# Kernel optimization log

Hardware: AMD Instinct MI355X
Metric: run time of the kernel (lower is better)

The kernel has to match this reference:

```python
import jax, jax.numpy as jnp
import numpy as np
import math

ATTN_TEMP = 1.0


def bilinear_sample(fea, gx, gy):
    """fea: [B,C,Hs,Ws]; gx, gy: [B,N] pixel coords (align_corners=True), zero padding."""
    B, C, Hs, Ws = fea.shape
    x0 = jnp.floor(gx)
    y0 = jnp.floor(gy)
    x1 = x0 + 1.0
    y1 = y0 + 1.0
    wx1 = gx - x0
    wx0 = 1.0 - wx1
    wy1 = gy - y0
    wy0 = 1.0 - wy1
    flat = fea.reshape(B, C, Hs * Ws)

    def gather(xi, yi, w):
        valid = (xi >= 0) & (xi <= Ws - 1) & (yi >= 0) & (yi <= Hs - 1)
        xi_c = jnp.clip(xi, 0, Ws - 1).astype(jnp.int32)
        yi_c = jnp.clip(yi, 0, Hs - 1).astype(jnp.int32)
        idx = yi_c * Ws + xi_c  # [B,N]
        vals = jnp.take_along_axis(flat, idx[:, None, :], axis=2)  # [B,C,N]
        return vals * (w * valid.astype(fea.dtype))[:, None, :]

    return (gather(x0, y0, wx0 * wy0) + gather(x1, y0, wx1 * wy0)
            + gather(x0, y1, wx0 * wy1) + gather(x1, y1, wx1 * wy1))


def homo_warp(src_fea, src_proj, ref_proj, depth_values):
    """Plane-sweep homography warp. src_fea [B,C,Hs,Ws], projs [B,4,4], depth [B,D,Hr,Wr]."""
    B, C, Hs, Ws = src_fea.shape
    _, D, Hr, Wr = depth_values.shape
    proj = src_proj @ jnp.linalg.inv(ref_proj)
    rot = proj[:, :3, :3]
    trans = proj[:, :3, 3]  # [B,3]
    y, x = jnp.meshgrid(jnp.arange(Hr, dtype=src_fea.dtype),
                        jnp.arange(Wr, dtype=src_fea.dtype), indexing='ij')
    ones = jnp.ones(Hr * Wr, dtype=src_fea.dtype)
    xyz = jnp.stack([x.ravel(), y.ravel(), ones])  # [3,N]
    rot_xyz = jnp.einsum('bij,jn->bin', rot, xyz)  # [B,3,N]
    # [B,3,D,N]
    proj_xyz = rot_xyz[:, :, None, :] * depth_values.reshape(B, 1, D, Hr * Wr) \
               + trans[:, :, None, None]
    z = proj_xyz[:, 2]
    z = jnp.where(z == 0, jnp.asarray(1e-9, z.dtype), z)
    px = (proj_xyz[:, 0] / z).reshape(B, -1)  # pixel coords (equivalent to normalize+align_corners)
    py = (proj_xyz[:, 1] / z).reshape(B, -1)
    warped = bilinear_sample(src_fea, px, py)  # [B,C,D*Hr*Wr]
    return warped.reshape(B, C, D, Hr, Wr)


def make_proj(p):
    """p: [B,2,4,4] (extrinsic, intrinsic) -> combined [B,4,4]."""
    top = jnp.einsum('bij,bjk->bik', p[:, 1, :3, :3], p[:, 0, :3, :4])
    return p[:, 0].at[:, :3, :4].set(top)


def setup_inputs() -> dict:
    key = jax.random.key(0)
    k1, k2, k3 = jax.random.split(key, 3)
    V, B, C, H, W, D, G = 5, 2, 32, 128, 128, 32, 8
    features = jax.random.normal(k1, (V, B, C, H, W), dtype=jnp.float32)
    rng = np.random.default_rng(0)
    ext = np.tile(np.eye(4, dtype=np.float32), (B, V, 1, 1))
    ext[..., :3, :3] += 0.01 * rng.normal(size=(B, V, 3, 3)).astype(np.float32)
    ext[..., :3, 3] += 0.1 * rng.normal(size=(B, V, 3)).astype(np.float32)
    intr = np.tile(np.eye(4, dtype=np.float32), (B, V, 1, 1))
    intr[..., 0, 0] = 600.0
    intr[..., 1, 1] = 600.0
    intr[..., 0, 2] = W / 2.0
    intr[..., 1, 2] = H / 2.0
    proj_matrices = jnp.asarray(np.stack([ext, intr], axis=2))  # [B,V,2,4,4]
    base = jnp.linspace(425.0, 935.0, D, dtype=jnp.float32)[None, :, None, None]
    depth_hypo = base + 2.0 * jax.random.uniform(k2, (B, D, H, W), dtype=jnp.float32)
    reg_w = jax.random.normal(k3, (G,), dtype=jnp.float32)
    return {"features": features, "proj_matrices": proj_matrices,
            "depth_hypo": depth_hypo, "reg_w": reg_w}


def reference(features, proj_matrices, depth_hypo, reg_w):
    V = features.shape[0]
    ref_feature = features[0]
    B, C, H, W = ref_feature.shape
    D = depth_hypo.shape[1]
    G = reg_w.shape[0]
    ref_proj = make_proj(proj_matrices[:, 0])
    ref_vol = ref_feature.reshape(B, G, C // G, 1, H, W)
    dh_ng = jax.lax.stop_gradient(depth_hypo)  # warp grid is no_grad in torch
    cor_weight_sum = 1e-8
    cor_feats = 0.0
    inv_sqrt_c = 1.0 / math.sqrt(C)
    for v in range(1, V):
        src_proj = make_proj(proj_matrices[:, v])
        warped = homo_warp(features[v], jax.lax.stop_gradient(src_proj),
                           jax.lax.stop_gradient(ref_proj), dh_ng)
        # group correlation: [B,G,D,H,W]
        cor_feat = (warped.reshape(B, G, C // G, D, H, W) * ref_vol).mean(2)
        cor_weight = jax.nn.softmax(cor_feat.sum(1) / ATTN_TEMP, axis=1) * inv_sqrt_c
        cor_weight_sum = cor_weight_sum + cor_weight
        cor_feats = cor_feats + cor_weight[:, None] * cor_feat
    cor_feats = cor_feats / cor_weight_sum[:, None]
    logits = jnp.einsum('g,bgdhw->bdhw', reg_w, cor_feats)  # regnet stand-in
    attn_weight = jax.nn.softmax(logits, axis=1)
    idx = jnp.argmax(attn_weight, axis=1, keepdims=True)  # [B,1,H,W]
    depth = jnp.take_along_axis(depth_hypo, idx, axis=1)[:, 0]  # [B,H,W]
    return depth, attn_weight
```

## Files before the change

kernel.cpp:

```cpp
#include <hip/hip_runtime.h>
#include <math.h>

#pragma clang fp contract(off)

#define VV 5
#define BB 2
#define CC 32
#define HH 128
#define WW 128
#define DD 32
#define GG 8
#define HWW (HH*WW)
#define TRBLOCKS (VV*BB*(HWW/64))

typedef float v2f __attribute__((ext_vector_type(2)));

__global__ __launch_bounds__(256) void prep_kernel(const float* __restrict__ fea,
                                                   float* __restrict__ featT,
                                                   const float* __restrict__ pm,
                                                   float* __restrict__ wproj) {
#pragma clang fp contract(off)
    int t = threadIdx.x;
    if (blockIdx.x == TRBLOCKS) {
        int tid = t;
        if (tid >= BB * (VV - 1)) return;
        int b = tid / (VV - 1);
        int v = tid % (VV - 1) + 1;

        float refP[4][4], srcP[4][4];
        for (int which = 0; which < 2; which++) {
            int view = (which == 0) ? 0 : v;
            const float* base = pm + (size_t)(b * VV + view) * 2 * 16;
            const float* ext  = base;
            const float* intr = base + 16;
            float (*M)[4] = (which == 0) ? refP : srcP;
            for (int r = 0; r < 3; r++)
                for (int c = 0; c < 4; c++) {
                    float s = 0.f;
                    for (int k = 0; k < 3; k++)
                        s = fmaf(intr[r * 4 + k], ext[k * 4 + c], s);
                    M[r][c] = s;
                }
            for (int c = 0; c < 4; c++) M[3][c] = ext[12 + c];
        }

        float A[4][4];
        for (int r = 0; r < 4; r++)
            for (int c = 0; c < 4; c++) A[r][c] = refP[r][c];
        int ipiv[4];
        for (int j = 0; j < 4; j++) {
            int p = j; float amax = fabsf(A[j][j]);
            for (int i = j + 1; i < 4; i++) {
                float tt = fabsf(A[i][j]);
                if (tt > amax) { amax = tt; p = i; }
            }
            ipiv[j] = p;
            if (p != j)
                for (int c = 0; c < 4; c++) { float tt = A[j][c]; A[j][c] = A[p][c]; A[p][c] = tt; }
            float rcp = 1.0f / A[j][j];
            for (int i = j + 1; i < 4; i++) A[i][j] = A[i][j] * rcp;
            for (int i = j + 1; i < 4; i++)
                for (int k = j + 1; k < 4; k++)
                    A[i][k] = fmaf(-A[i][j], A[j][k], A[i][k]);
        }

        float Bm[4][4];
        for (int r = 0; r < 4; r++)
            for (int c = 0; c < 4; c++) Bm[r][c] = (r == c) ? 1.f : 0.f;
        for (int j = 0; j < 4; j++) {
            int p = ipiv[j];
            if (p != j)
                for (int c = 0; c < 4; c++) { float tt = Bm[j][c]; Bm[j][c] = Bm[p][c]; Bm[p][c] = tt; }
        }
        float invd[4];
        for (int k = 0; k < 4; k++) invd[k] = 1.0f / A[k][k];
        for (int c = 0; c < 4; c++) {
            for (int k = 0; k < 4; k++)
                for (int i = k + 1; i < 4; i++)
                    Bm[i][c] = fmaf(-A[i][k], Bm[k][c], Bm[i][c]);
            for (int k = 3; k >= 0; k--) {
                Bm[k][c] = Bm[k][c] * invd[k];
                for (int i = 0; i < k; i++)
                    Bm[i][c] = fmaf(-A[i][k], Bm[k][c], Bm[i][c]);
            }
        }

        float P[3][4];
        for (int r = 0; r < 3; r++)
            for (int c = 0; c < 4; c++) {
                float s = 0.f;
                for (int k = 0; k < 4; k++)
                    s = fmaf(srcP[r][k], Bm[k][c], s);
                P[r][c] = s;
            }
        float* o = wproj + (b * (VV - 1) + (v - 1)) * 12;
        for (int r = 0; r < 3; r++)
            for (int c = 0; c < 3; c++) o[r * 3 + c] = P[r][c];
        for (int r = 0; r < 3; r++) o[9 + r] = P[r][3];
        return;
    }

    __shared__ float tile[64][36];
    int vb = blockIdx.x >> 8;
    int base = (blockIdx.x & 255) * 64;
#pragma unroll
    for (int k = 0; k < 2; k++) {
        int c = (t >> 4) + 16 * k;
        int p = t & 15;
        float4 v = *(const float4*)&fea[((size_t)vb * CC + c) * HWW + base + 4 * p];
        int cs = c ^ ((p & 7) << 2);
        tile[4 * p + 0][cs] = v.x;
        tile[4 * p + 1][cs] = v.y;
        tile[4 * p + 2][cs] = v.z;
        tile[4 * p + 3][cs] = v.w;
    }
    __syncthreads();
#pragma unroll
    for (int m = 0; m < 2; m++) {
        int pl = (t >> 3) + 32 * m;
        int q = t & 7;
        int sw = ((pl >> 2) & 7) << 2;
        float4 v = *(const float4*)&tile[pl][(4 * q) ^ sw];
        *(float4*)&featT[((size_t)vb * HWW + base + pl) * CC + 4 * q] = v;
    }
}

__global__ __launch_bounds__(256) void main_kernel(const float* __restrict__ featT,
                                                   const float* __restrict__ wproj,
                                                   const float* __restrict__ depth_hypo,
                                                   const float* __restrict__ reg_w,
                                                   float* __restrict__ out) {
#pragma clang fp contract(off)
    __shared__ float s_ref[8][32];
    __shared__ float s_e[8][32];
    __shared__ float s_proj[4][12];
    __shared__ float s_regw[8];

    int t = threadIdx.x;
    int d = t & 31, pl = t >> 5;
    int base = t & 32;
    int pixbase = blockIdx.x * 8;
    int b = pixbase / HWW;
    int hwb = pixbase - b * HWW;

    s_ref[pl][d] = featT[((size_t)(b * HWW + hwb + pl)) * CC + d];
    if (t < 48) s_proj[t / 12][t % 12] = wproj[b * (VV - 1) * 12 + t];
    if (t < 8) s_regw[t] = reg_w[t];
    __syncthreads();

    int hw = hwb + pl;
    int y = hw >> 7, x = hw & (WW - 1);
    float fx = (float)x, fy = (float)y;
    float dep = depth_hypo[(size_t)(b * DD + d) * HWW + hw];

    v2f refv[16];
#pragma unroll
    for (int g = 0; g < 8; g++) {
        float4 r = *(const float4*)&s_ref[pl][g * 4];
        refv[2 * g]     = (v2f){r.x, r.y};
        refv[2 * g + 1] = (v2f){r.z, r.w};
    }

    float accs[8];
#pragma unroll
    for (int g = 0; g < 8; g++) accs[g] = 0.f;
    float cws = 1e-8f;

    for (int vi = 0; vi < 4; vi++) {
        const float* pr = s_proj[vi];
        float rx = fmaf(pr[1], fy, pr[0] * fx) + pr[2];
        float ry = fmaf(pr[4], fy, pr[3] * fx) + pr[5];
        float rz = fmaf(pr[7], fy, pr[6] * fx) + pr[8];
        float X = rx * dep + pr[9];
        float Y = ry * dep + pr[10];
        float Z = rz * dep + pr[11];
        if (Z == 0.f) Z = 1e-9f;
        float px = X / Z, py = Y / Z;

        float x0f = floorf(px), y0f = floorf(py);
        float x1f = x0f + 1.0f, y1f = y0f + 1.0f;
        float wx1 = px - x0f, wx0 = 1.0f - wx1;
        float wy1 = py - y0f, wy0 = 1.0f - wy1;
        bool vx0 = (x0f >= 0.f) && (x0f <= (float)(WW - 1));
        bool vx1 = (x1f >= 0.f) && (x1f <= (float)(WW - 1));
        bool vy0 = (y0f >= 0.f) && (y0f <= (float)(HH - 1));
        bool vy1 = (y1f >= 0.f) && (y1f <= (float)(HH - 1));

        int xc0 = (int)fminf(fmaxf(x0f, 0.f), (float)(WW - 1));
        int xc1 = (int)fminf(fmaxf(x1f, 0.f), (float)(WW - 1));
        int yc0 = (int)fminf(fmaxf(y0f, 0.f), (float)(HH - 1));
        int yc1 = (int)fminf(fmaxf(y1f, 0.f), (float)(HH - 1));

        float w00 = (wx0 * wy0) * ((vx0 && vy0) ? 1.f : 0.f);
        float w10 = (wx1 * wy0) * ((vx1 && vy0) ? 1.f : 0.f);
        float w01 = (wx0 * wy1) * ((vx0 && vy1) ? 1.f : 0.f);
        float w11 = (wx1 * wy1) * ((vx1 && vy1) ? 1.f : 0.f);

        v2f w00v = (v2f){w00, w00};
        v2f w10v = (v2f){w10, w10};
        v2f w01v = (v2f){w01, w01};
        v2f w11v = (v2f){w11, w11};

        const float* srcB = featT + (size_t)((vi + 1) * BB + b) * HWW * CC;
        const float4* p00 = (const float4*)(srcB + ((size_t)yc0 * WW + xc0) * CC);
        const float4* p10 = (const float4*)(srcB + ((size_t)yc0 * WW + xc1) * CC);
        const float4* p01 = (const float4*)(srcB + ((size_t)yc1 * WW + xc0) * CC);
        const float4* p11 = (const float4*)(srcB + ((size_t)yc1 * WW + xc1) * CC);

        float cf[8];
        float s = 0.f;
#pragma unroll
        for (int g = 0; g < 8; g++) {
            float4 f00 = p00[g], f10 = p10[g], f01 = p01[g], f11 = p11[g];
            v2f f00l = (v2f){f00.x, f00.y}, f00h = (v2f){f00.z, f00.w};
            v2f f10l = (v2f){f10.x, f10.y}, f10h = (v2f){f10.z, f10.w};
            v2f f01l = (v2f){f01.x, f01.y}, f01h = (v2f){f01.z, f01.w};
            v2f f11l = (v2f){f11.x, f11.y}, f11h = (v2f){f11.z, f11.w};

            v2f a = f00l * w00v;
            a = a + f10l * w10v;
            a = a + f01l * w01v;
            a = a + f11l * w11v;
            v2f bq = f00h * w00v;
            bq = bq + f10h * w10v;
            bq = bq + f01h * w01v;
            bq = bq + f11h * w11v;

            v2f prl = a * refv[2 * g];
            v2f prh = bq * refv[2 * g + 1];

            float gs = prl.x;
            gs = gs + prl.y; gs = gs + prh.x; gs = gs + prh.y;
            gs = gs * 0.25f;
            cf[g] = gs;
            s = s + gs;
        }

        float m = s;
#pragma unroll
        for (int msk = 1; msk < 32; msk <<= 1) m = fmaxf(m, __shfl_xor(m, msk, 64));
        float e = expf(s - m);
        s_e[pl][d] = e;
        float sum = 0.f;
#pragma unroll
        for (int j = 0; j < 8; j++) {
            float4 q = *(const float4*)&s_e[pl][j * 4];
            sum = sum + q.x; sum = sum + q.y; sum = sum + q.z; sum = sum + q.w;
        }
        float cw = (e / sum) * 0.17677669529663687f;

        cws = cws + cw;
#pragma unroll
        for (int g = 0; g < 8; g++) {
            float tterm = cw * cf[g];
            accs[g] = accs[g] + tterm;
        }
    }

    float logit = 0.f;
#pragma unroll
    for (int g = 0; g < 8; g++) {
        float cfn = accs[g] / cws;
        logit = fmaf(s_regw[g], cfn, logit);
    }

    float m2 = logit;
#pragma unroll
    for (int msk = 1; msk < 32; msk <<= 1) m2 = fmaxf(m2, __shfl_xor(m2, msk, 64));
    float e2 = expf(logit - m2);
    s_e[pl][d] = e2;
    float s2 = 0.f;
#pragma unroll
    for (int j = 0; j < 8; j++) {
        float4 q = *(const float4*)&s_e[pl][j * 4];
        s2 = s2 + q.x; s2 = s2 + q.y; s2 = s2 + q.z; s2 = s2 + q.w;
    }
    float attn = e2 / s2;
    out[(size_t)BB * HWW + (size_t)(b * DD + d) * HWW + hw] = attn;

    float a1 = attn;
#pragma unroll
    for (int msk = 1; msk < 32; msk <<= 1) a1 = fmaxf(a1, __shfl_xor(a1, msk, 64));
    int idx1 = (attn == a1) ? d : 1000;
#pragma unroll
    for (int msk = 1; msk < 32; msk <<= 1) {
        int oi = __shfl_xor(idx1, msk, 64);
        idx1 = (oi < idx1) ? oi : idx1;
    }
    float dep1 = __shfl(dep, base + idx1, 64);
    if (d == 0) out[b * HWW + hw] = dep1;
}

extern "C" void kernel_launch(void* const* d_in, const int* in_sizes, int n_in,
                              void* d_out, int out_size, void* d_ws, size_t ws_size,
                              hipStream_t stream) {
    const float* features   = (const float*)d_in[0];
    const float* pm         = (const float*)d_in[1];
    const float* depth_hypo = (const float*)d_in[2];
    const float* reg_w      = (const float*)d_in[3];
    float* out = (float*)d_out;

    float* wproj = (float*)d_ws;
    float* featT = (float*)((char*)d_ws + 4096);

    prep_kernel<<<TRBLOCKS + 1, 256, 0, stream>>>(features, featT, pm, wproj);
    main_kernel<<<BB * HWW / 8, 256, 0, stream>>>(featT, wproj, depth_hypo, reg_w, out);
}
```

Before: 152.6 us.

## Parallelize source views across warps and combine via shared memory

Each block now handles 2 pixels instead of 8, and each group of 32 threads processes one source view rather than looping over all four views in sequence. Per-view correlation features and softmax weights are written to shared memory and reduced after a barrier. This exposes four independent gather chains per pixel to increase memory-level parallelism and latency hiding. The cost is a 4x larger grid, more shared-memory traffic, redundant final softmax and argmax work in the three non-writing view groups, and an added occupancy hint.

After: 166.8 us. 1.09x slower.

```diff
diff --git a/kernel.cpp b/kernel.cpp
--- a/kernel.cpp
+++ b/kernel.cpp
@@ -125,134 +125,142 @@
     }
 }
 
-__global__ __launch_bounds__(256) void main_kernel(const float* __restrict__ featT,
-                                                   const float* __restrict__ wproj,
-                                                   const float* __restrict__ depth_hypo,
-                                                   const float* __restrict__ reg_w,
-                                                   float* __restrict__ out) {
+__global__ __launch_bounds__(256, 8) void main_kernel(const float* __restrict__ featT,
+                                                      const float* __restrict__ wproj,
+                                                      const float* __restrict__ depth_hypo,
+                                                      const float* __restrict__ reg_w,
+                                                      float* __restrict__ out) {
 #pragma clang fp contract(off)
-    __shared__ float s_ref[8][32];
+    __shared__ float s_ref[2][32];
     __shared__ float s_e[8][32];
     __shared__ float s_proj[4][12];
     __shared__ float s_regw[8];
+    __shared__ float s_cw[2][4][32];
+    __shared__ float s_cf[2][4][8][32];
 
     int t = threadIdx.x;
-    int d = t & 31, pl = t >> 5;
+    int d   = t & 31;
+    int vi  = (t >> 5) & 3;
+    int pxl = t >> 7;
+    int row = t >> 5;
     int base = t & 32;
-    int pixbase = blockIdx.x * 8;
+
+    int pixbase = blockIdx.x * 2;
     int b = pixbase / HWW;
     int hwb = pixbase - b * HWW;
 
-    s_ref[pl][d] = featT[((size_t)(b * HWW + hwb + pl)) * CC + d];
+    if (t < 64) s_ref[t >> 5][t & 31] = featT[((size_t)(b * HWW + hwb + (t >> 5))) * CC + (t & 31)];
     if (t < 48) s_proj[t / 12][t % 12] = wproj[b * (VV - 1) * 12 + t];
     if (t < 8) s_regw[t] = reg_w[t];
     __syncthreads();
 
-    int hw = hwb + pl;
+    int hw = hwb + pxl;
     int y = hw >> 7, x = hw & (WW - 1);
     float fx = (float)x, fy = (float)y;
     float dep = depth_hypo[(size_t)(b * DD + d) * HWW + hw];
 
-    v2f refv[16];
+    const float* pr = s_proj[vi];
+    float rx = fmaf(pr[1], fy, pr[0] * fx) + pr[2];
+    float ry = fmaf(pr[4], fy, pr[3] * fx) + pr[5];
+    float rz = fmaf(pr[7], fy, pr[6] * fx) + pr[8];
+    float X = rx * dep + pr[9];
+    float Y = ry * dep + pr[10];
+    float Z = rz * dep + pr[11];
+    if (Z == 0.f) Z = 1e-9f;
+    float px = X / Z, py = Y / Z;
+
+    float x0f = floorf(px), y0f = floorf(py);
+    float x1f = x0f + 1.0f, y1f = y0f + 1.0f;
+    float wx1 = px - x0f, wx0 = 1.0f - wx1;
+    float wy1 = py - y0f, wy0 = 1.0f - wy1;
+    bool vx0 = (x0f >= 0.f) && (x0f <= (float)(WW - 1));
+    bool vx1 = (x1f >= 0.f) && (x1f <= (float)(WW - 1));
+    bool vy0 = (y0f >= 0.f) && (y0f <= (float)(HH - 1));
+    bool vy1 = (y1f >= 0.f) && (y1f <= (float)(HH - 1));
+
+    int xc0 = (int)fminf(fmaxf(x0f, 0.f), (float)(WW - 1));
+    int xc1 = (int)fminf(fmaxf(x1f, 0.f), (float)(WW - 1));
+    int yc0 = (int)fminf(fmaxf(y0f, 0.f), (float)(HH - 1));
+    int yc1 = (int)fminf(fmaxf(y1f, 0.f), (float)(HH - 1));
+
+    float w00 = (wx0 * wy0) * ((vx0 && vy0) ? 1.f : 0.f);
+    float w10 = (wx1 * wy0) * ((vx1 && vy0) ? 1.f : 0.f);
+    float w01 = (wx0 * wy1) * ((vx0 && vy1) ? 1.f : 0.f);
+    float w11 = (wx1 * wy1) * ((vx1 && vy1) ? 1.f : 0.f);
+
+    v2f w00v = (v2f){w00, w00};
+    v2f w10v = (v2f){w10, w10};
+    v2f w01v = (v2f){w01, w01};
+    v2f w11v = (v2f){w11, w11};
+
+    const float* srcB = featT + (size_t)((vi + 1) * BB + b) * HWW * CC;
+    const float4* p00 = (const float4*)(srcB + ((size_t)yc0 * WW + xc0) * CC);
+    const float4* p10 = (const float4*)(srcB + ((size_t)yc0 * WW + xc1) * CC);
+    const float4* p01 = (const float4*)(srcB + ((size_t)yc1 * WW + xc0) * CC);
+    const float4* p11 = (const float4*)(srcB + ((size_t)yc1 * WW + xc1) * CC);
+
+    float cf[8];
+    float s = 0.f;
 #pragma unroll
     for (int g = 0; g < 8; g++) {
-        float4 r = *(const float4*)&s_ref[pl][g * 4];
-        refv[2 * g]     = (v2f){r.x, r.y};
-        refv[2 * g + 1] = (v2f){r.z, r.w};
-    }
-
+        float4 f00 = p00[g], f10 = p10[g], f01 = p01[g], f11 = p11[g];
+        v2f f00l = (v2f){f00.x, f00.y}, f00h = (v2f){f00.z, f00.w};
+        v2f f10l = (v2f){f10.x, f10.y}, f10h = (v2f){f10.z, f10.w};
+        v2f f01l = (v2f){f01.x, f01.y}, f01h = (v2f){f01.z, f01.w};
+        v2f f11l = (v2f){f11.x, f11.y}, f11h = (v2f){f11.z, f11.w};
+
+        v2f a = f00l * w00v;
+        a = a + f10l * w10v;
+        a = a + f01l * w01v;
+        a = a + f11l * w11v;
+        v2f bq = f00h * w00v;
+        bq = bq + f10h * w10v;
+        bq = bq + f01h * w01v;
+        bq = bq + f11h * w11v;
+
+        float4 r4 = *(const float4*)&s_ref[pxl][g * 4];
+        v2f refl = (v2f){r4.x, r4.y};
+        v2f refh = (v2f){r4.z, r4.w};
+
+        v2f prl = a * refl;
+        v2f prh = bq * refh;
+
+        float gs = prl.x;
+        gs = gs + prl.y; gs = gs + prh.x; gs = gs + prh.y;
+        gs = gs * 0.25f;
+        cf[g] = gs;
+        s = s + gs;
+    }
+
+    float m = s;
+#pragma unroll
+    for (int msk = 1; msk < 32; msk <<= 1) m = fmaxf(m, __shfl_xor(m, msk, 64));
+    float e = expf(s - m);
+    s_e[row][d] = e;
+    float sum = 0.f;
+#pragma unroll
+    for (int j = 0; j < 8; j++) {
+        float4 q = *(const float4*)&s_e[row][j * 4];
+        sum = sum + q.x; sum = sum + q.y; sum = sum + q.z; sum = sum + q.w;
+    }
+    float cw = (e / sum) * 0.17677669529663687f;
+
+    s_cw[pxl][vi][d] = cw;
+#pragma unroll
+    for (int g = 0; g < 8; g++) s_cf[pxl][vi][g][d] = cf[g];
+    __syncthreads();
+
+    float cws = 1e-8f;
     float accs[8];
 #pragma unroll
     for (int g = 0; g < 8; g++) accs[g] = 0.f;
-    float cws = 1e-8f;
-
-    for (int vi = 0; vi < 4; vi++) {
-        const float* pr = s_proj[vi];
-        float rx = fmaf(pr[1], fy, pr[0] * fx) + pr[2];
-        float ry = fmaf(pr[4], fy, pr[3] * fx) + pr[5];
-        float rz = fmaf(pr[7], fy, pr[6] * fx) + pr[8];
-        float X = rx * dep + pr[9];
-        float Y = ry * dep + pr[10];
-        float Z = rz * dep + pr[11];
-        if (Z == 0.f) Z = 1e-9f;
-        float px = X / Z, py = Y / Z;
-
-        float x0f = floorf(px), y0f = floorf(py);
-        float x1f = x0f + 1.0f, y1f = y0f + 1.0f;
-        float wx1 = px - x0f, wx0 = 1.0f - wx1;
-        float wy1 = py - y0f, wy0 = 1.0f - wy1;
-        bool vx0 = (x0f >= 0.f) && (x0f <= (float)(WW - 1));
-        bool vx1 = (x1f >= 0.f) && (x1f <= (float)(WW - 1));
-        bool vy0 = (y0f >= 0.f) && (y0f <= (float)(HH - 1));
-        bool vy1 = (y1f >= 0.f) && (y1f <= (float)(HH - 1));
-
-        int xc0 = (int)fminf(fmaxf(x0f, 0.f), (float)(WW - 1));
-        int xc1 = (int)fminf(fmaxf(x1f, 0.f), (float)(WW - 1));
-        int yc0 = (int)fminf(fmaxf(y0f, 0.f), (float)(HH - 1));
-        int yc1 = (int)fminf(fmaxf(y1f, 0.f), (float)(HH - 1));
-
-        float w00 = (wx0 * wy0) * ((vx0 && vy0) ? 1.f : 0.f);
-        float w10 = (wx1 * wy0) * ((vx1 && vy0) ? 1.f : 0.f);
-        float w01 = (wx0 * wy1) * ((vx0 && vy1) ? 1.f : 0.f);
-        float w11 = (wx1 * wy1) * ((vx1 && vy1) ? 1.f : 0.f);
-
-        v2f w00v = (v2f){w00, w00};
-        v2f w10v = (v2f){w10, w10};
-        v2f w01v = (v2f){w01, w01};
-        v2f w11v = (v2f){w11, w11};
-
-        const float* srcB = featT + (size_t)((vi + 1) * BB + b) * HWW * CC;
-        const float4* p00 = (const float4*)(srcB + ((size_t)yc0 * WW + xc0) * CC);
-        const float4* p10 = (const float4*)(srcB + ((size_t)yc0 * WW + xc1) * CC);
-        const float4* p01 = (const float4*)(srcB + ((size_t)yc1 * WW + xc0) * CC);
-        const float4* p11 = (const float4*)(srcB + ((size_t)yc1 * WW + xc1) * CC);
-
-        float cf[8];
-        float s = 0.f;
+#pragma unroll
+    for (int v = 0; v < 4; v++) {
+        float cwv = s_cw[pxl][v][d];
+        cws = cws + cwv;
 #pragma unroll
         for (int g = 0; g < 8; g++) {
-            float4 f00 = p00[g], f10 = p10[g], f01 = p01[g], f11 = p11[g];
-            v2f f00l = (v2f){f00.x, f00.y}, f00h = (v2f){f00.z, f00.w};
-            v2f f10l = (v2f){f10.x, f10.y}, f10h = (v2f){f10.z, f10.w};
-            v2f f01l = (v2f){f01.x, f01.y}, f01h = (v2f){f01.z, f01.w};
-            v2f f11l = (v2f){f11.x, f11.y}, f11h = (v2f){f11.z, f11.w};
-
-            v2f a = f00l * w00v;
-            a = a + f10l * w10v;
-            a = a + f01l * w01v;
-            a = a + f11l * w11v;
-            v2f bq = f00h * w00v;
-            bq = bq + f10h * w10v;
-            bq = bq + f01h * w01v;
-            bq = bq + f11h * w11v;
-
-            v2f prl = a * refv[2 * g];
-            v2f prh = bq * refv[2 * g + 1];
-
-            float gs = prl.x;
-            gs = gs + prl.y; gs = gs + prh.x; gs = gs + prh.y;
-            gs = gs * 0.25f;
-            cf[g] = gs;
-            s = s + gs;
-        }
-
-        float m = s;
-#pragma unroll
-        for (int msk = 1; msk < 32; msk <<= 1) m = fmaxf(m, __shfl_xor(m, msk, 64));
-        float e = expf(s - m);
-        s_e[pl][d] = e;
-        float sum = 0.f;
-#pragma unroll
-        for (int j = 0; j < 8; j++) {
-            float4 q = *(const float4*)&s_e[pl][j * 4];
-            sum = sum + q.x; sum = sum + q.y; sum = sum + q.z; sum = sum + q.w;
-        }
-        float cw = (e / sum) * 0.17677669529663687f;
-
-        cws = cws + cw;
-#pragma unroll
-        for (int g = 0; g < 8; g++) {
-            float tterm = cw * cf[g];
+            float tterm = cwv * s_cf[pxl][v][g][d];
             accs[g] = accs[g] + tterm;
         }
     }
@@ -268,15 +276,15 @@
 #pragma unroll
     for (int msk = 1; msk < 32; msk <<= 1) m2 = fmaxf(m2, __shfl_xor(m2, msk, 64));
     float e2 = expf(logit - m2);
-    s_e[pl][d] = e2;
+    s_e[row][d] = e2;
     float s2 = 0.f;
 #pragma unroll
     for (int j = 0; j < 8; j++) {
-        float4 q = *(const float4*)&s_e[pl][j * 4];
+        float4 q = *(const float4*)&s_e[row][j * 4];
         s2 = s2 + q.x; s2 = s2 + q.y; s2 = s2 + q.z; s2 = s2 + q.w;
     }
     float attn = e2 / s2;
-    out[(size_t)BB * HWW + (size_t)(b * DD + d) * HWW + hw] = attn;
+    if (vi == 0) out[(size_t)BB * HWW + (size_t)(b * DD + d) * HWW + hw] = attn;
 
     float a1 = attn;
 #pragma unroll
@@ -288,7 +296,7 @@
         idx1 = (oi < idx1) ? oi : idx1;
     }
     float dep1 = __shfl(dep, base + idx1, 64);
-    if (d == 0) out[b * HWW + hw] = dep1;
+    if (vi == 0 && d == 0) out[b * HWW + hw] = dep1;
 }
 
 extern "C" void kernel_launch(void* const* d_in, const int* in_sizes, int n_in,
@@ -304,5 +312,5 @@
     float* featT = (float*)((char*)d_ws + 4096);
 
     prep_kernel<<<TRBLOCKS + 1, 256, 0, stream>>>(features, featT, pm, wproj);
-    main_kernel<<<BB * HWW / 8, 256, 0, stream>>>(featT, wproj, depth_hypo, reg_w, out);
+    main_kernel<<<BB * HWW / 2, 256, 0, stream>>>(featT, wproj, depth_hypo, reg_w, out);
 }
```
